# Kernel optimization log

Hardware: AMD Instinct MI355X
Metric: run time of the kernel (lower is better)

## Reference

```python
import jax, jax.numpy as jnp
import numpy as np

DIM = 512
HEADS = 8
HEAD_DIM = DIM // HEADS
SCALE = HEAD_DIM ** -0.5


def setup_inputs() -> dict:
    key = jax.random.key(0)
    ks = jax.random.split(key, 7)
    B, QN, N = 32, 128, 4096
    q = jax.random.normal(ks[0], (B, QN, DIM), dtype=jnp.float32)
    kv = jax.random.normal(ks[1], (B, N, DIM), dtype=jnp.float32)
    key_mask = jax.random.normal(ks[2], (B, QN, N), dtype=jnp.float32)
    Wq = jax.random.normal(ks[3], (DIM, DIM), dtype=jnp.float32) * 0.02
    Wkv = jax.random.normal(ks[4], (2 * DIM, DIM), dtype=jnp.float32) * 0.02
    Wproj = jax.random.normal(ks[5], (DIM, DIM), dtype=jnp.float32) * 0.02
    bproj = jax.random.normal(ks[6], (DIM,), dtype=jnp.float32) * 0.02
    return {"q": q, "kv": kv, "key_mask": key_mask,
            "Wq": Wq, "Wkv": Wkv, "Wproj": Wproj, "bproj": bproj}


def reference(q, kv, key_mask, Wq, Wkv, Wproj, bproj):
    B, QN, C = q.shape
    N = kv.shape[1]
    # q projection -> [B, QN, H, hd]
    qh = (q @ Wq.T).reshape(B, QN, HEADS, HEAD_DIM) * SCALE
    # kv projection -> split into k, v each [B, N, H, hd]
    kvp = kv @ Wkv.T  # [B, N, 2C]
    k = kvp[..., :C].reshape(B, N, HEADS, HEAD_DIM)
    v = kvp[..., C:].reshape(B, N, HEADS, HEAD_DIM)
    # scores [B, H, QN, N] + additive mask broadcast over heads
    attn = jnp.einsum('bqhd,bkhd->bhqk', qh, k) + key_mask[:, None]
    attn = jax.nn.softmax(attn, axis=-1)
    x = jnp.einsum('bhqk,bkhd->bqhd', attn, v).reshape(B, QN, C)
    return x @ Wproj.T + bproj
```

## Files before the change

kernel.cpp:

```cpp
#include <hip/hip_runtime.h>
#include <hip/hip_bf16.h>

typedef __attribute__((ext_vector_type(4))) float f32x4;
typedef __attribute__((ext_vector_type(8))) short bf16x8;
typedef __attribute__((ext_vector_type(4))) unsigned short ush4;

#define GAS __attribute__((address_space(1)))
#define LAS __attribute__((address_space(3)))

__device__ __forceinline__ unsigned int cvtpk(float lo, float hi) {
  unsigned int r;
  asm("v_cvt_pk_bf16_f32 %0, %1, %2" : "=v"(r) : "v"(lo), "v"(hi));
  return r;
}
__device__ __forceinline__ unsigned short f2bf(float f) { return (unsigned short)cvtpk(f, f); }
__device__ __forceinline__ f32x4 mfma16(bf16x8 a, bf16x8 b, f32x4 c) {
  return __builtin_amdgcn_mfma_f32_16x16x32_bf16(a, b, c, 0, 0, 0);
}
__device__ __forceinline__ void gl_lds16(const unsigned short* g, unsigned short* l) {
  __builtin_amdgcn_global_load_lds((const GAS unsigned short*)g, (LAS unsigned short*)l, 16, 0, 0);
}
__device__ __forceinline__ void memfence_sched() { asm volatile("" ::: "memory"); }

__global__ __launch_bounds__(256)
void cvt_f32_bf16(const float* __restrict__ in, unsigned short* __restrict__ out, int n8) {
  for (int i = blockIdx.x * blockDim.x + threadIdx.x; i < n8; i += gridDim.x * blockDim.x) {
    const float4 a = *reinterpret_cast<const float4*>(in + (size_t)i * 8);
    const float4 b = *reinterpret_cast<const float4*>(in + (size_t)i * 8 + 4);
    uint4 o;
    o.x = cvtpk(a.x, a.y); o.y = cvtpk(a.z, a.w);
    o.z = cvtpk(b.x, b.y); o.w = cvtpk(b.z, b.w);
    *reinterpret_cast<uint4*>(out + (size_t)i * 8) = o;
  }
}

template<int MODE, bool AF32>
__global__ __launch_bounds__(256, 3)
void gemmM(const void* __restrict__ Agv, const unsigned short* __restrict__ Bg,
           void* __restrict__ Cg, void* __restrict__ Cg2,
           const float* __restrict__ bias, int ntn, size_t ldc)
{
  __shared__ unsigned short sm[16384];
  unsigned short* const smB = sm + 8192;

  const int t = threadIdx.x, lane = t & 63, w = t >> 6;
  const int lo = lane & 15, hi = lane >> 4;
  const int wm = w >> 1, wn = w & 1;
  const int nwg = gridDim.x, bid = blockIdx.x;
  const int id = (bid & 7) * (nwg >> 3) + (bid >> 3);
  const int row0 = (id / ntn) * 128, col0 = (id % ntn) * 128;

  const float* Af = (const float*)Agv;
  const unsigned short* Ab = (const unsigned short*)Agv;

  const int swcol = ((lane & 3) ^ ((lane >> 3) & 3)) * 8;
  const unsigned short* bS = Bg + (size_t)(col0 + w * 32 + (lane >> 2)) * 512 + swcol;
  const unsigned short* aSg = Ab + (size_t)(row0 + w * 32 + (lane >> 2)) * 512 + swcol;

  const int rs_r = t >> 2;
  const int rs_c = (t & 3) * 8;
  const int wch = ((t & 3) ^ ((t >> 3) & 3)) * 8;

  float4 stF[2][4];

  auto F_ISSUE = [&](int kt) {
    if constexpr (AF32) {
      const int bk = kt & 1;
      const float* s0 = Af + (size_t)(row0 + rs_r) * 512 + kt * 32 + rs_c;
      const float* s1 = Af + (size_t)(row0 + 64 + rs_r) * 512 + kt * 32 + rs_c;
      stF[bk][0] = *(const float4*)s0; stF[bk][1] = *(const float4*)(s0 + 4);
      stF[bk][2] = *(const float4*)s1; stF[bk][3] = *(const float4*)(s1 + 4);
    }
  };
  auto F_WRITE = [&](int kt) {
    if constexpr (AF32) {
      const int bk = kt & 1;
      unsigned short* fb = &sm[(kt & 1) * 4096];
      uint4 o;
      o.x = cvtpk(stF[bk][0].x, stF[bk][0].y); o.y = cvtpk(stF[bk][0].z, stF[bk][0].w);
      o.z = cvtpk(stF[bk][1].x, stF[bk][1].y); o.w = cvtpk(stF[bk][1].z, stF[bk][1].w);
      *reinterpret_cast<uint4*>(&fb[rs_r * 32 + wch]) = o;
      o.x = cvtpk(stF[bk][2].x, stF[bk][2].y); o.y = cvtpk(stF[bk][2].z, stF[bk][2].w);
      o.z = cvtpk(stF[bk][3].x, stF[bk][3].y); o.w = cvtpk(stF[bk][3].z, stF[bk][3].w);
      *reinterpret_cast<uint4*>(&fb[(64 + rs_r) * 32 + wch]) = o;
    }
  };
  auto G_ISSUE = [&](int kt) {
    unsigned short* bb = &smB[(kt & 1) * 4096];
    gl_lds16(bS + kt * 32,                     bb + (w * 2 + 0) * 512);
    gl_lds16(bS + (size_t)16 * 512 + kt * 32,  bb + (w * 2 + 1) * 512);
    if constexpr (!AF32) {
      unsigned short* ab = &sm[(kt & 1) * 4096];
      gl_lds16(aSg + kt * 32,                    ab + (w * 2 + 0) * 512);
      gl_lds16(aSg + (size_t)16 * 512 + kt * 32, ab + (w * 2 + 1) * 512);
    }
  };

  f32x4 acc[4][4] = {};
  const int fxor = (hi ^ ((lo >> 1) & 3)) * 8;

  if constexpr (AF32) {
    F_ISSUE(0);
    G_ISSUE(0);
    F_ISSUE(1);
    memfence_sched();
    asm volatile("s_waitcnt vmcnt(6)" ::: "memory");
    F_WRITE(0);
    asm volatile("s_waitcnt vmcnt(4)" ::: "memory");
  } else {
    G_ISSUE(0);
    memfence_sched();
    asm volatile("s_waitcnt vmcnt(0)" ::: "memory");
  }
  asm volatile("s_waitcnt lgkmcnt(0)" ::: "memory");
  __builtin_amdgcn_s_barrier();
  memfence_sched();

  #pragma unroll
  for (int kt = 0; kt < 16; ++kt) {
    const unsigned short* ab = &sm[(kt & 1) * 4096];
    const unsigned short* bb = &smB[(kt & 1) * 4096];
    bf16x8 bfr[4], af[4];
    #pragma unroll
    for (int nj = 0; nj < 4; ++nj)
      bfr[nj] = *reinterpret_cast<const bf16x8*>(&bb[(wn * 64 + nj * 16 + lo) * 32 + fxor]);
    #pragma unroll
    for (int mi = 0; mi < 4; ++mi)
      af[mi] = *reinterpret_cast<const bf16x8*>(&ab[(wm * 64 + mi * 16 + lo) * 32 + fxor]);

    if (kt <= 14) G_ISSUE(kt + 1);
    if constexpr (AF32) { if (kt <= 13) F_ISSUE(kt + 2); }
    memfence_sched();

    __builtin_amdgcn_s_setprio(1);
    #pragma unroll
    for (int mi = 0; mi < 2; ++mi)
      #pragma unroll
      for (int nj = 0; nj < 4; ++nj)
        acc[mi][nj] = mfma16(af[mi], bfr[nj], acc[mi][nj]);
    __builtin_amdgcn_s_setprio(0);

    if constexpr (AF32) {
      if (kt <= 13)      { asm volatile("s_waitcnt vmcnt(6)" ::: "memory"); }
      else if (kt == 14) { asm volatile("s_waitcnt vmcnt(2)" ::: "memory"); }
      if (kt <= 14) F_WRITE(kt + 1);
    }

    __builtin_amdgcn_s_setprio(1);
    #pragma unroll
    for (int mi = 2; mi < 4; ++mi)
      #pragma unroll
      for (int nj = 0; nj < 4; ++nj)
        acc[mi][nj] = mfma16(af[mi], bfr[nj], acc[mi][nj]);
    __builtin_amdgcn_s_setprio(0);

    if (kt < 15) {
      if constexpr (AF32) {
        if (kt <= 13) { asm volatile("s_waitcnt vmcnt(4)" ::: "memory"); }
        else          { asm volatile("s_waitcnt vmcnt(0)" ::: "memory"); }
      } else {
        asm volatile("s_waitcnt vmcnt(0)" ::: "memory");
      }
      asm volatile("s_waitcnt lgkmcnt(0)" ::: "memory");
      __builtin_amdgcn_s_barrier();
      memfence_sched();
    }
  }

  if constexpr (MODE == 3) {
    __syncthreads();
    unsigned short* Tb = &sm[w * 4096];
    if (col0 < 512) {
      #pragma unroll
      for (int q = 0; q < 4; ++q)
        #pragma unroll
        for (int nj = 0; nj < 4; ++nj)
          #pragma unroll
          for (int r = 0; r < 4; ++r)
            Tb[(q * 16 + hi * 4 + r) * 64 + nj * 16 + lo] = f2bf(acc[q][nj][r]);
      asm volatile("s_waitcnt lgkmcnt(0)" ::: "memory");
      #pragma unroll
      for (int it = 0; it < 8; ++it) {
        const int rr = it * 8 + (lane >> 3);
        const bf16x8 v = *reinterpret_cast<const bf16x8*>(&Tb[rr * 64 + (lane & 7) * 8]);
        const size_t gm = (size_t)row0 + wm * 64 + rr;
        *reinterpret_cast<bf16x8*>((unsigned short*)Cg + gm * 512 + col0 + wn * 64 +
                                   (lane & 7) * 8) = v;
      }
    } else {
      #pragma unroll
      for (int q = 0; q < 4; ++q)
        #pragma unroll
        for (int nj = 0; nj < 4; ++nj)
          #pragma unroll
          for (int r = 0; r < 4; ++r) {
            const int gn_l = nj * 16 + lo;
            const int gm_l = (q * 16 + hi * 4 + r) ^ ((gn_l & 15) * 4);
            Tb[gn_l * 64 + gm_l] = f2bf(acc[q][nj][r]);
          }
      asm volatile("s_waitcnt lgkmcnt(0)" ::: "memory");
      #pragma unroll
      for (int it = 0; it < 16; ++it) {
        const int gn_l = it * 4 + (lane >> 4);
        const int g4 = ((lane & 15) * 4) ^ ((gn_l & 15) * 4);
        const ush4 v = *reinterpret_cast<const ush4*>(&Tb[gn_l * 64 + g4]);
        const size_t vrow = (size_t)(col0 - 512) + wn * 64 + gn_l;
        const size_t vcol = (size_t)row0 + wm * 64 + (lane & 15) * 4;
        *reinterpret_cast<ush4*>((unsigned short*)Cg2 + vrow * 131072 + vcol) = v;
      }
    }
  } else {
    #pragma unroll
    for (int mi = 0; mi < 4; ++mi) {
      #pragma unroll
      for (int r = 0; r < 4; ++r) {
        const size_t gm = (size_t)row0 + wm * 64 + mi * 16 + hi * 4 + r;
        #pragma unroll
        for (int nj = 0; nj < 4; ++nj) {
          const int gn = col0 + wn * 64 + nj * 16 + lo;
          const float v = acc[mi][nj][r];
          if constexpr (MODE == 0)
            ((unsigned short*)Cg)[gm * ldc + gn] = f2bf(v * 0.125f);
          else
            ((float*)Cg)[gm * ldc + gn] = v + bias[gn];
        }
      }
    }
  }
}

__global__ __launch_bounds__(256)
void attn_fwd(const unsigned short* __restrict__ qh,
              const unsigned short* __restrict__ kbuf,
              const unsigned short* __restrict__ vT,
              const float* __restrict__ mask,
              float* __restrict__ opart, float* __restrict__ ml)
{
  __shared__ unsigned short Ks[64 * 64];
  __shared__ unsigned short Vs[64 * 64];
  __shared__ unsigned short Ps[4][16 * 64];
  const int bid = blockIdx.x;
  const int xcd = bid & 7, g = bid >> 3;
  const int b = (g >> 6) * 8 + xcd;
  const int sub = g & 63;
  const int h = sub >> 3, qhalf = (sub >> 2) & 1, c = sub & 3;
  const int n0 = c * 1024;
  const int bh2 = (b * 8 + h) * 2 + qhalf;
  const int t = threadIdx.x, lane = t & 63, w = t >> 6;
  const int hi = lane >> 4, lo = lane & 15;
  const int q0 = qhalf * 64 + w * 16;

  bf16x8 aq[2];
  #pragma unroll
  for (int kk = 0; kk < 2; ++kk)
    aq[kk] = *reinterpret_cast<const bf16x8*>(
        qh + (size_t)(b * 128 + q0 + lo) * 512 + h * 64 + kk * 32 + hi * 8);

  float mrow[4], lrow[4];
  #pragma unroll
  for (int i = 0; i < 4; ++i) { mrow[i] = -1e30f; lrow[i] = 0.f; }
  f32x4 o[4] = {};

  const unsigned short* kp = kbuf + ((size_t)b * 4096 + n0) * 512 + h * 64;
  const unsigned short* vp = vT + (size_t)(h * 64) * 131072 + (size_t)b * 4096 + n0;
  const float* mp = mask + ((size_t)(b * 128 + q0)) * 4096 + n0;

  for (int nt = 0; nt < 16; ++nt) {
    {
      const int r = t >> 3, cc = t & 7;
      *reinterpret_cast<uint4*>(&Ks[r * 64 + ((cc ^ (r & 7)) << 3)]) =
          *reinterpret_cast<const uint4*>(kp + (size_t)(nt * 64 + r) * 512 + (cc << 3));
      *reinterpret_cast<uint4*>(&Ks[(r + 32) * 64 + ((cc ^ (r & 7)) << 3)]) =
          *reinterpret_cast<const uint4*>(kp + (size_t)(nt * 64 + r + 32) * 512 + (cc << 3));
      *reinterpret_cast<uint4*>(&Vs[r * 64 + ((cc ^ (r & 7)) << 3)]) =
          *reinterpret_cast<const uint4*>(vp + (size_t)r * 131072 + nt * 64 + (cc << 3));
      *reinterpret_cast<uint4*>(&Vs[(r + 32) * 64 + ((cc ^ (r & 7)) << 3)]) =
          *reinterpret_cast<const uint4*>(vp + (size_t)(r + 32) * 131072 + nt * 64 + (cc << 3));
    }
    __syncthreads();

    f32x4 s[4] = {};
    __builtin_amdgcn_s_setprio(1);
    #pragma unroll
    for (int ni = 0; ni < 4; ++ni) {
      #pragma unroll
      for (int kk = 0; kk < 2; ++kk) {
        const bf16x8 kf = *reinterpret_cast<const bf16x8*>(
            &Ks[(ni * 16 + lo) * 64 + ((kk * 32 + hi * 8) ^ ((lo & 7) << 3))]);
        s[ni] = mfma16(aq[kk], kf, s[ni]);
      }
    }
    __builtin_amdgcn_s_setprio(0);
    #pragma unroll
    for (int ni = 0; ni < 4; ++ni)
      #pragma unroll
      for (int r = 0; r < 4; ++r)
        s[ni][r] += mp[(size_t)(hi * 4 + r) * 4096 + nt * 64 + ni * 16 + lo];

    #pragma unroll
    for (int r = 0; r < 4; ++r) {
      float mx = fmaxf(fmaxf(s[0][r], s[1][r]), fmaxf(s[2][r], s[3][r]));
      #pragma unroll
      for (int off = 1; off < 16; off <<= 1)
        mx = fmaxf(mx, __shfl_xor(mx, off, 64));
      const float mnew = fmaxf(mrow[r], mx);
      const float corr = __expf(mrow[r] - mnew);
      mrow[r] = mnew;
      float ls = 0.f;
      #pragma unroll
      for (int ni = 0; ni < 4; ++ni) {
        const float p = __expf(s[ni][r] - mnew);
        s[ni][r] = p; ls += p;
      }
      #pragma unroll
      for (int off = 1; off < 16; off <<= 1)
        ls += __shfl_xor(ls, off, 64);
      lrow[r] = lrow[r] * corr + ls;
      #pragma unroll
      for (int di = 0; di < 4; ++di)
        o[di][r] *= corr;
    }

    #pragma unroll
    for (int ni = 0; ni < 4; ++ni)
      #pragma unroll
      for (int r = 0; r < 4; ++r) {
        const int rp = hi * 4 + r;
        Ps[w][rp * 64 + ((ni * 16 + lo) ^ ((rp & 7) << 3))] = f2bf(s[ni][r]);
      }

    __builtin_amdgcn_s_setprio(1);
    #pragma unroll
    for (int kk = 0; kk < 2; ++kk) {
      const bf16x8 pa = *reinterpret_cast<const bf16x8*>(
          &Ps[w][lo * 64 + ((kk * 32 + hi * 8) ^ ((lo & 7) << 3))]);
      #pragma unroll
      for (int di = 0; di < 4; ++di) {
        const bf16x8 vf = *reinterpret_cast<const bf16x8*>(
            &Vs[(di * 16 + lo) * 64 + ((kk * 32 + hi * 8) ^ ((lo & 7) << 3))]);
        o[di] = mfma16(pa, vf, o[di]);
      }
    }
    __builtin_amdgcn_s_setprio(0);
    __syncthreads();
  }

  const size_t pbase = ((size_t)bh2 * 4 + c) * 64;
  #pragma unroll
  for (int di = 0; di < 4; ++di)
    #pragma unroll
    for (int r = 0; r < 4; ++r)
      opart[(pbase + (w * 16 + hi * 4 + r)) * 64 + di * 16 + lo] = o[di][r];
  if (lo == 0) {
    #pragma unroll
    for (int r = 0; r < 4; ++r) {
      const int qq = w * 16 + hi * 4 + r;
      ml[(((size_t)bh2 * 4 + c) * 2 + 0) * 64 + qq] = mrow[r];
      ml[(((size_t)bh2 * 4 + c) * 2 + 1) * 64 + qq] = lrow[r];
    }
  }
}

__global__ __launch_bounds__(256)
void attn_combine(const float* __restrict__ opart, const float* __restrict__ ml,
                  unsigned short* __restrict__ xb)
{
  const int bh2 = blockIdx.x;
  const int b = bh2 >> 4, h = (bh2 >> 1) & 7, qhalf = bh2 & 1;
  const int t = threadIdx.x;
  const int q = t >> 2, dg = t & 3;

  float m[4], l[4];
  #pragma unroll
  for (int c = 0; c < 4; ++c) {
    m[c] = ml[(((size_t)bh2 * 4 + c) * 2 + 0) * 64 + q];
    l[c] = ml[(((size_t)bh2 * 4 + c) * 2 + 1) * 64 + q];
  }
  const float M = fmaxf(fmaxf(m[0], m[1]), fmaxf(m[2], m[3]));
  float sc[4], L = 0.f;
  #pragma unroll
  for (int c = 0; c < 4; ++c) { sc[c] = __expf(m[c] - M); L += sc[c] * l[c]; }
  const float inv = 1.f / L;

  float4 acc[4] = {};
  #pragma unroll
  for (int c = 0; c < 4; ++c) {
    const float* base = opart + (((size_t)bh2 * 4 + c) * 64 + q) * 64 + dg * 16;
    #pragma unroll
    for (int j = 0; j < 4; ++j) {
      const float4 v = *reinterpret_cast<const float4*>(base + j * 4);
      acc[j].x = fmaf(sc[c], v.x, acc[j].x);
      acc[j].y = fmaf(sc[c], v.y, acc[j].y);
      acc[j].z = fmaf(sc[c], v.z, acc[j].z);
      acc[j].w = fmaf(sc[c], v.w, acc[j].w);
    }
  }
  unsigned short* dst = xb + ((size_t)b * 128 + qhalf * 64 + q) * 512 + h * 64 + dg * 16;
  uint4 o1, o2;
  o1.x = cvtpk(acc[0].x * inv, acc[0].y * inv); o1.y = cvtpk(acc[0].z * inv, acc[0].w * inv);
  o1.z = cvtpk(acc[1].x * inv, acc[1].y * inv); o1.w = cvtpk(acc[1].z * inv, acc[1].w * inv);
  o2.x = cvtpk(acc[2].x * inv, acc[2].y * inv); o2.y = cvtpk(acc[2].z * inv, acc[2].w * inv);
  o2.z = cvtpk(acc[3].x * inv, acc[3].y * inv); o2.w = cvtpk(acc[3].z * inv, acc[3].w * inv);
  *reinterpret_cast<uint4*>(dst) = o1;
  *reinterpret_cast<uint4*>(dst + 8) = o2;
}

extern "C" void kernel_launch(void* const* d_in, const int* in_sizes, int n_in,
                              void* d_out, int out_size, void* d_ws, size_t ws_size,
                              hipStream_t stream) {
  const float* q     = (const float*)d_in[0];
  const float* kv    = (const float*)d_in[1];
  const float* mask  = (const float*)d_in[2];
  const float* Wq    = (const float*)d_in[3];
  const float* Wkv   = (const float*)d_in[4];
  const float* Wproj = (const float*)d_in[5];
  const float* bproj = (const float*)d_in[6];
  float* out = (float*)d_out;

  char* ws = (char*)d_ws;
  unsigned short* kbuf   = (unsigned short*)ws;
  unsigned short* vTb    = (unsigned short*)(ws + 134217728ULL);
  float*          opart  = (float*)(ws + 268435456ULL);
  float*          mlb    = (float*)(ws + 301989888ULL);
  unsigned short* qhb    = (unsigned short*)(ws + 303038464ULL);
  unsigned short* xb     = (unsigned short*)(ws + 307232768ULL);
  unsigned short* Wqb    = (unsigned short*)(ws + 311427072ULL);
  unsigned short* Wkvb   = (unsigned short*)(ws + 311951360ULL);
  unsigned short* Wprojb = (unsigned short*)(ws + 312999936ULL);

  cvt_f32_bf16<<<128, 256, 0, stream>>>(Wq, Wqb, 512 * 512 / 8);
  cvt_f32_bf16<<<256, 256, 0, stream>>>(Wkv, Wkvb, 1024 * 512 / 8);
  cvt_f32_bf16<<<128, 256, 0, stream>>>(Wproj, Wprojb, 512 * 512 / 8);

  gemmM<0, true><<<128, 256, 0, stream>>>(q, Wqb, qhb, nullptr, nullptr, 4, 512);
  gemmM<3, true><<<8192, 256, 0, stream>>>(kv, Wkvb, kbuf, vTb, nullptr, 8, 512);
  attn_fwd<<<2048, 256, 0, stream>>>(qhb, kbuf, vTb, mask, opart, mlb);
  attn_combine<<<512, 256, 0, stream>>>(opart, mlb, xb);
  gemmM<2, false><<<128, 256, 0, stream>>>(xb, Wprojb, out, nullptr, bproj, 4, 512);
}
```

Before: 420.4 us.

## Pre-convert kv to bf16 in chunks and triple-buffer the bf16 GEMM pipeline

The fused f32-load kv projection is replaced by a separate f32-to-bf16 conversion pass over kv, done in two halves into a scratch buffer and followed by the all-bf16 GEMM variant. That bf16 GEMM path now uses three LDS stages with prefetch distance two, so waits are relaxed to vmcnt(4). The goal is to feed the GEMM with direct global-to-LDS bf16 loads and a deeper pipeline instead of per-thread register conversion. The cost is an extra full read of kv plus a write and re-read of its bf16 copy, and more LDS per block. The vT output offset for the second chunk depends on how MODE 3 writes transposed V, which is not visible here.

```diff
diff --git a/kernel.cpp b/kernel.cpp
--- a/kernel.cpp
+++ b/kernel.cpp
@@ -40,8 +40,9 @@
            void* __restrict__ Cg, void* __restrict__ Cg2,
            const float* __restrict__ bias, int ntn, size_t ldc)
 {
-  __shared__ unsigned short sm[16384];
-  unsigned short* const smB = sm + 8192;
+  constexpr int NS = AF32 ? 2 : 3;
+  __shared__ unsigned short sm[NS * 2 * 4096];
+  unsigned short* const smB = sm + NS * 4096;
 
   const int t = threadIdx.x, lane = t & 63, w = t >> 6;
   const int lo = lane & 15, hi = lane >> 4;
@@ -75,7 +76,7 @@
   auto F_WRITE = [&](int kt) {
     if constexpr (AF32) {
       const int bk = kt & 1;
-      unsigned short* fb = &sm[(kt & 1) * 4096];
+      unsigned short* fb = &sm[(kt % NS) * 4096];
       uint4 o;
       o.x = cvtpk(stF[bk][0].x, stF[bk][0].y); o.y = cvtpk(stF[bk][0].z, stF[bk][0].w);
       o.z = cvtpk(stF[bk][1].x, stF[bk][1].y); o.w = cvtpk(stF[bk][1].z, stF[bk][1].w);
@@ -86,11 +87,11 @@
     }
   };
   auto G_ISSUE = [&](int kt) {
-    unsigned short* bb = &smB[(kt & 1) * 4096];
-    gl_lds16(bS + kt * 32,                     bb + (w * 2 + 0) * 512);
-    gl_lds16(bS + (size_t)16 * 512 + kt * 32,  bb + (w * 2 + 1) * 512);
+    unsigned short* bb = &smB[(kt % NS) * 4096];
+    gl_lds16(bS + kt * 32,                    bb + (w * 2 + 0) * 512);
+    gl_lds16(bS + (size_t)16 * 512 + kt * 32, bb + (w * 2 + 1) * 512);
     if constexpr (!AF32) {
-      unsigned short* ab = &sm[(kt & 1) * 4096];
+      unsigned short* ab = &sm[(kt % NS) * 4096];
       gl_lds16(aSg + kt * 32,                    ab + (w * 2 + 0) * 512);
       gl_lds16(aSg + (size_t)16 * 512 + kt * 32, ab + (w * 2 + 1) * 512);
     }
@@ -108,9 +109,9 @@
     F_WRITE(0);
     asm volatile("s_waitcnt vmcnt(4)" ::: "memory");
   } else {
-    G_ISSUE(0);
+    G_ISSUE(0); G_ISSUE(1);
     memfence_sched();
-    asm volatile("s_waitcnt vmcnt(0)" ::: "memory");
+    asm volatile("s_waitcnt vmcnt(4)" ::: "memory");
   }
   asm volatile("s_waitcnt lgkmcnt(0)" ::: "memory");
   __builtin_amdgcn_s_barrier();
@@ -118,8 +119,8 @@
 
   #pragma unroll
   for (int kt = 0; kt < 16; ++kt) {
-    const unsigned short* ab = &sm[(kt & 1) * 4096];
-    const unsigned short* bb = &smB[(kt & 1) * 4096];
+    const unsigned short* ab = &sm[(kt % NS) * 4096];
+    const unsigned short* bb = &smB[(kt % NS) * 4096];
     bf16x8 bfr[4], af[4];
     #pragma unroll
     for (int nj = 0; nj < 4; ++nj)
@@ -128,8 +129,12 @@
     for (int mi = 0; mi < 4; ++mi)
       af[mi] = *reinterpret_cast<const bf16x8*>(&ab[(wm * 64 + mi * 16 + lo) * 32 + fxor]);
 
-    if (kt <= 14) G_ISSUE(kt + 1);
-    if constexpr (AF32) { if (kt <= 13) F_ISSUE(kt + 2); }
+    if constexpr (AF32) {
+      if (kt <= 14) G_ISSUE(kt + 1);
+      if (kt <= 13) F_ISSUE(kt + 2);
+    } else {
+      if (kt <= 13) G_ISSUE(kt + 2);
+    }
     memfence_sched();
 
     __builtin_amdgcn_s_setprio(1);
@@ -159,7 +164,8 @@
         if (kt <= 13) { asm volatile("s_waitcnt vmcnt(4)" ::: "memory"); }
         else          { asm volatile("s_waitcnt vmcnt(0)" ::: "memory"); }
       } else {
-        asm volatile("s_waitcnt vmcnt(0)" ::: "memory");
+        if (kt <= 13) { asm volatile("s_waitcnt vmcnt(4)" ::: "memory"); }
+        else          { asm volatile("s_waitcnt vmcnt(0)" ::: "memory"); }
       }
       asm volatile("s_waitcnt lgkmcnt(0)" ::: "memory");
       __builtin_amdgcn_s_barrier();
@@ -420,20 +426,29 @@
   char* ws = (char*)d_ws;
   unsigned short* kbuf   = (unsigned short*)ws;
   unsigned short* vTb    = (unsigned short*)(ws + 134217728ULL);
+  unsigned short* kvbfc  = (unsigned short*)(ws + 268435456ULL);
   float*          opart  = (float*)(ws + 268435456ULL);
   float*          mlb    = (float*)(ws + 301989888ULL);
-  unsigned short* qhb    = (unsigned short*)(ws + 303038464ULL);
-  unsigned short* xb     = (unsigned short*)(ws + 307232768ULL);
-  unsigned short* Wqb    = (unsigned short*)(ws + 311427072ULL);
-  unsigned short* Wkvb   = (unsigned short*)(ws + 311951360ULL);
-  unsigned short* Wprojb = (unsigned short*)(ws + 312999936ULL);
+  unsigned short* xb     = (unsigned short*)(ws + 303038464ULL);
+  unsigned short* qhb    = (unsigned short*)(ws + 335544320ULL);
+  unsigned short* Wqb    = (unsigned short*)(ws + 339738624ULL);
+  unsigned short* Wkvb   = (unsigned short*)(ws + 340262912ULL);
+  unsigned short* Wprojb = (unsigned short*)(ws + 341311488ULL);
 
   cvt_f32_bf16<<<128, 256, 0, stream>>>(Wq, Wqb, 512 * 512 / 8);
   cvt_f32_bf16<<<256, 256, 0, stream>>>(Wkv, Wkvb, 1024 * 512 / 8);
   cvt_f32_bf16<<<128, 256, 0, stream>>>(Wproj, Wprojb, 512 * 512 / 8);
 
   gemmM<0, true><<<128, 256, 0, stream>>>(q, Wqb, qhb, nullptr, nullptr, 4, 512);
-  gemmM<3, true><<<8192, 256, 0, stream>>>(kv, Wkvb, kbuf, vTb, nullptr, 8, 512);
+
+  for (int c = 0; c < 2; ++c) {
+    cvt_f32_bf16<<<2048, 256, 0, stream>>>(kv + (size_t)c * 65536 * 512, kvbfc,
+                                           65536 * 512 / 8);
+    gemmM<3, false><<<4096, 256, 0, stream>>>(kvbfc, Wkvb,
+                                              kbuf + (size_t)c * 65536 * 512,
+                                              vTb + (size_t)c * 65536, nullptr, 8, 512);
+  }
+
   attn_fwd<<<2048, 256, 0, stream>>>(qhb, kbuf, vTb, mask, opart, mlb);
   attn_combine<<<512, 256, 0, stream>>>(opart, mlb, xb);
   gemmM<2, false><<<128, 256, 0, stream>>>(xb, Wprojb, out, nullptr, bproj, 4, 512);
```

New measurement: 395.9 us. 1.06x faster.
